# Performance work log

Measured on AMD Instinct MI355X. Metric: run time of the kernel, lower is better.

## Reference

```python
import jax, jax.numpy as jnp
import numpy as np

CHEB_K = 3

def setup_inputs() -> dict:
    key = jax.random.key(0)
    k1, k2, k3, k4 = jax.random.split(key, 4)
    B, N, C_IN, C_OUT, D = 64, 2048, 64, 64, 16
    return {
        "x": jax.random.normal(k1, (B, N, C_IN), dtype=jnp.float32),
        "node_embeddings": jax.random.normal(k2, (N, D), dtype=jnp.float32),
        "weights_pool": jax.random.normal(k3, (D, CHEB_K, C_IN, C_OUT), dtype=jnp.float32) * 0.1,
        "bias_pool": jax.random.normal(k4, (D, C_OUT), dtype=jnp.float32) * 0.1,
    }

def reference(x, node_embeddings, weights_pool, bias_pool):
    # x: [B, N, C_in]; node_embeddings: [N, D]
    N = node_embeddings.shape[0]
    # adaptive adjacency: row-softmax of relu(E E^T)
    supports = jax.nn.softmax(jax.nn.relu(node_embeddings @ node_embeddings.T), axis=1)
    # Chebyshev polynomial recursion: T0 = I, T1 = A, Tk = 2 A T_{k-1} - T_{k-2}
    support_set = [jnp.eye(N, dtype=x.dtype), supports]
    for _ in range(2, CHEB_K):
        support_set.append(2.0 * supports @ support_set[-1] - support_set[-2])
    supports_stack = jnp.stack(support_set, axis=0)  # [K, N, N]
    # per-node generated weights/bias from embedding pools
    weights = jnp.einsum('nd,dkio->nkio', node_embeddings, weights_pool)  # [N, K, C_in, C_out]
    bias = node_embeddings @ bias_pool  # [N, C_out]
    # graph convolution: aggregate then per-node GEMM
    x_g = jnp.einsum('knm,bmc->bknc', supports_stack, x)  # [B, K, N, C_in]
    out = jnp.einsum('bkni,nkio->bno', x_g, weights) + bias  # [B, N, C_out]
    return out
```

## Files before the change

kernel.cpp:

```cpp
#include <hip/hip_runtime.h>
#include <hip/hip_bf16.h>
#include <stdint.h>

using bf16   = __bf16;
using bf16x8 = __attribute__((ext_vector_type(8))) __bf16;
using f32x4  = __attribute__((ext_vector_type(4))) float;

#define NN  2048
#define DD  16
#define BB  64
#define CC  64
#define BCC 4096
#define GNODE 2

__device__ inline float4 f4max(float4 a, float4 b) {
  return make_float4(fmaxf(a.x,b.x), fmaxf(a.y,b.y), fmaxf(a.z,b.z), fmaxf(a.w,b.w));
}
__device__ inline float4 f4add(float4 a, float4 b) {
  return make_float4(a.x+b.x, a.y+b.y, a.z+b.z, a.w+b.w);
}

__global__ __launch_bounds__(256) void k_softmax(const float* __restrict__ E,
                                                 bf16* __restrict__ A) {
  const int n0 = blockIdx.x * 4;
  const int t = threadIdx.x;
  float en[4][DD];
#pragma unroll
  for (int g = 0; g < 4; ++g)
#pragma unroll
    for (int d = 0; d < DD; ++d) en[g][d] = E[(size_t)(n0 + g) * DD + d];

  float4 r[8];
  float4 mx = make_float4(0.f, 0.f, 0.f, 0.f);
#pragma unroll
  for (int j = 0; j < 8; ++j) {
    const int m = t + 256 * j;
    const float4* ep = (const float4*)(E + (size_t)m * DD);
    float4 p0 = ep[0], p1 = ep[1], p2 = ep[2], p3 = ep[3];
    float s[4];
#pragma unroll
    for (int g = 0; g < 4; ++g) {
      s[g] = p0.x*en[g][0] + p0.y*en[g][1] + p0.z*en[g][2] + p0.w*en[g][3]
           + p1.x*en[g][4] + p1.y*en[g][5] + p1.z*en[g][6] + p1.w*en[g][7]
           + p2.x*en[g][8] + p2.y*en[g][9] + p2.z*en[g][10] + p2.w*en[g][11]
           + p3.x*en[g][12]+ p3.y*en[g][13]+ p3.z*en[g][14]+ p3.w*en[g][15];
      s[g] = fmaxf(s[g], 0.0f);
    }
    r[j] = make_float4(s[0], s[1], s[2], s[3]);
    mx = f4max(mx, r[j]);
  }
  __shared__ float4 red[256];
  red[t] = mx;
  __syncthreads();
  for (int off = 128; off > 0; off >>= 1) {
    if (t < off) red[t] = f4max(red[t], red[t + off]);
    __syncthreads();
  }
  mx = red[0];
  __syncthreads();
  float4 ex[8];
  float4 sum = make_float4(0.f, 0.f, 0.f, 0.f);
#pragma unroll
  for (int j = 0; j < 8; ++j) {
    ex[j] = make_float4(__expf(r[j].x - mx.x), __expf(r[j].y - mx.y),
                        __expf(r[j].z - mx.z), __expf(r[j].w - mx.w));
    sum = f4add(sum, ex[j]);
  }
  red[t] = sum;
  __syncthreads();
  for (int off = 128; off > 0; off >>= 1) {
    if (t < off) red[t] = f4add(red[t], red[t + off]);
    __syncthreads();
  }
  const float4 tot = red[0];
  const float inv[4] = {1.f/tot.x, 1.f/tot.y, 1.f/tot.z, 1.f/tot.w};
#pragma unroll
  for (int j = 0; j < 8; ++j) {
    const int m = t + 256 * j;
    A[(size_t)(n0 + 0) * NN + m] = (bf16)(ex[j].x * inv[0]);
    A[(size_t)(n0 + 1) * NN + m] = (bf16)(ex[j].y * inv[1]);
    A[(size_t)(n0 + 2) * NN + m] = (bf16)(ex[j].z * inv[2]);
    A[(size_t)(n0 + 3) * NN + m] = (bf16)(ex[j].w * inv[3]);
  }
}

__global__ __launch_bounds__(256) void k_transpose(const bf16* __restrict__ in,
                                                   bf16* __restrict__ out,
                                                   int R, int C) {
  __shared__ bf16 tile[64 * 68];
  const int bx = blockIdx.x, by = blockIdx.y;
  const int t = threadIdx.x;
  const int r0 = by * 64, c0 = bx * 64;
#pragma unroll
  for (int j = 0; j < 16; ++j) {
    const int q = t + 256 * j;
    const int r = q >> 6, c = q & 63;
    tile[r * 68 + c] = in[(size_t)(r0 + r) * C + c0 + c];
  }
  __syncthreads();
#pragma unroll
  for (int j = 0; j < 16; ++j) {
    const int q = t + 256 * j;
    const int rr = q >> 6, cc = q & 63;
    out[(size_t)(c0 + rr) * R + r0 + cc] = tile[cc * 68 + rr];
  }
}

__global__ __launch_bounds__(256) void k_build_xrt(const float* __restrict__ x,
                                                   bf16* __restrict__ XrT) {
  __shared__ bf16 tile[64 * 68];
  const int b = blockIdx.x;
  const int m0 = blockIdx.y * 64;
  const int t = threadIdx.x;
#pragma unroll
  for (int j = 0; j < 16; ++j) {
    const int q = t + 256 * j;
    const int m = q >> 6, i = q & 63;
    tile[m * 68 + i] = (bf16)x[((size_t)b * NN + m0 + m) * CC + i];
  }
  __syncthreads();
#pragma unroll
  for (int j = 0; j < 16; ++j) {
    const int q = t + 256 * j;
    const int i = q >> 6, m = q & 63;
    XrT[((size_t)b * CC + i) * NN + m0 + m] = tile[m * 68 + i];
  }
}

__global__ __launch_bounds__(256) void k_prep_wpt(const float* __restrict__ Wp,
                                                  bf16* __restrict__ WpT) {
  const int e = blockIdx.x * 256 + threadIdx.x;
  const int r = e >> 6, o = e & 63;
  const size_t src = (size_t)(r >> 6) * 4096 + (size_t)(r & 63) * 64 + o;
#pragma unroll
  for (int d = 0; d < DD; ++d)
    WpT[(size_t)e * DD + d] = (bf16)Wp[(size_t)d * 12288 + src];
}

template <int EPI>
__global__ __launch_bounds__(256) void k_gemm_bt(const bf16* __restrict__ L,
                                                 const bf16* __restrict__ R,
                                                 bf16* __restrict__ C,
                                                 int M, int Nc, int K,
                                                 const float* __restrict__ Xext,
                                                 bf16* __restrict__ CT) {
  __shared__ uint4 lds[4096];
  const int t = threadIdx.x;
  const int lane = t & 63, w = t >> 6;
  const int wm = w & 1, wn = w >> 1;
  const int h = lane >> 4;

  const int nwg = gridDim.x * gridDim.y;
  const int bid = blockIdx.y * gridDim.x + blockIdx.x;
  const int cpx = nwg >> 3;
  const int swz = (bid & 7) * cpx + (bid >> 3);
  const int bx = swz % gridDim.x, by = swz / gridDim.x;

  const int m0 = by * 128, n0 = bx * 128;

  f32x4 acc[4][4];
  const f32x4 zz = {0.f, 0.f, 0.f, 0.f};
#pragma unroll
  for (int mt = 0; mt < 4; ++mt)
#pragma unroll
    for (int nt = 0; nt < 4; ++nt) acc[mt][nt] = zz;

  auto stage = [&](int buf, int kt) {
    uint4* base = lds + buf * 2048;
#pragma unroll
    for (int c = 0; c < 4; ++c) {
      const int q = t + 256 * c;
      const int row = q >> 3, col4 = q & 7;
      const int scol = col4 ^ (row & 7);
      const bf16* srcL = L + (size_t)(m0 + row) * K + kt + (scol << 3);
      const bf16* srcR = R + (size_t)(n0 + row) * K + kt + (scol << 3);
      __builtin_amdgcn_global_load_lds(srcL, &base[q & ~63], 16, 0, 0);
      __builtin_amdgcn_global_load_lds(srcR, &base[1024 + (q & ~63)], 16, 0, 0);
    }
  };

  auto compute = [&](int buf) {
    const bf16x8* Lsv = (const bf16x8*)(lds + buf * 2048);
    const bf16x8* Rsv = (const bf16x8*)(lds + buf * 2048 + 1024);
#pragma unroll
    for (int kk = 0; kk < 2; ++kk) {
      bf16x8 af[4], bfr[4];
#pragma unroll
      for (int mt = 0; mt < 4; ++mt) {
        const int row = wm * 64 + mt * 16 + (lane & 15);
        af[mt] = Lsv[(row << 3) | ((kk * 4 + h) ^ (row & 7))];
      }
#pragma unroll
      for (int nt = 0; nt < 4; ++nt) {
        const int row = wn * 64 + nt * 16 + (lane & 15);
        bfr[nt] = Rsv[(row << 3) | ((kk * 4 + h) ^ (row & 7))];
      }
#pragma unroll
      for (int mt = 0; mt < 4; ++mt)
#pragma unroll
        for (int nt = 0; nt < 4; ++nt)
          acc[mt][nt] = __builtin_amdgcn_mfma_f32_16x16x32_bf16(
              af[mt], bfr[nt], acc[mt][nt], 0, 0, 0);
    }
  };

  const int NT = K >> 6;
  stage(0, 0);
  int cur = 0;
  for (int ts = 0; ts < NT - 1; ++ts) {
    stage(cur ^ 1, (ts + 1) << 6);
    asm volatile("s_waitcnt vmcnt(8)" ::: "memory");
    __builtin_amdgcn_s_barrier();
    __builtin_amdgcn_sched_barrier(0);
    compute(cur);
    __builtin_amdgcn_s_barrier();
    __builtin_amdgcn_sched_barrier(0);
    cur ^= 1;
  }
  asm volatile("s_waitcnt vmcnt(0)" ::: "memory");
  __builtin_amdgcn_s_barrier();
  __builtin_amdgcn_sched_barrier(0);
  compute(cur);

#pragma unroll
  for (int mt = 0; mt < 4; ++mt)
#pragma unroll
    for (int nt = 0; nt < 4; ++nt)
#pragma unroll
      for (int r = 0; r < 4; ++r) {
        const int rg = m0 + wm * 64 + mt * 16 + 4 * h + r;
        const int cg = n0 + wn * 64 + nt * 16 + (lane & 15);
        float v = acc[mt][nt][r];
        if (EPI == 2) {
          const int b = cg >> 6, i = cg & 63;
          v = 2.0f * v - Xext[(((size_t)b * NN + rg) * CC) + i];
        }
        C[(size_t)rg * Nc + cg] = (bf16)v;
      }

  if (EPI == 1) {
    __syncthreads();
    bf16* T = (bf16*)lds;
#pragma unroll
    for (int mt = 0; mt < 4; ++mt)
#pragma unroll
      for (int nt = 0; nt < 4; ++nt)
#pragma unroll
        for (int r = 0; r < 4; ++r) {
          const int rloc = wm * 64 + mt * 16 + 4 * h + r;
          const int cloc = wn * 64 + nt * 16 + (lane & 15);
          T[cloc * 136 + rloc] = (bf16)acc[mt][nt][r];
        }
    __syncthreads();
    const int cloc = t >> 1, half = t & 1;
#pragma unroll
    for (int jj = 0; jj < 8; ++jj) {
      const bf16x8 v = *(const bf16x8*)(T + cloc * 136 + half * 64 + jj * 8);
      *(bf16x8*)(CT + (size_t)(n0 + cloc) * M + m0 + half * 64 + jj * 8) = v;
    }
  }
}

__global__ __launch_bounds__(256) void k_node(const float* __restrict__ x,
                                              const float* __restrict__ E,
                                              const bf16* __restrict__ WpT,
                                              const float* __restrict__ bp,
                                              const bf16* __restrict__ xg1,
                                              const bf16* __restrict__ xg2,
                                              float* __restrict__ out) {
  __shared__ alignas(16) bf16 sW[GNODE * 1536 * 8];
  const int t = threadIdx.x;
  const int lane = t & 63, w = t >> 6;
  const int h = lane >> 4, l16 = lane & 15;
  const int n0 = blockIdx.x * GNODE;
  const int b = w * 16 + l16;

  float4  xa[GNODE][4];
  bf16x8  xgr[GNODE][4];
#pragma unroll
  for (int g = 0; g < GNODE; ++g) {
    const int n = n0 + g;
    const float* xb = x + ((size_t)b * NN + n) * CC;
    xa[g][0] = *(const float4*)(xb + h * 8);
    xa[g][1] = *(const float4*)(xb + h * 8 + 4);
    xa[g][2] = *(const float4*)(xb + 32 + h * 8);
    xa[g][3] = *(const float4*)(xb + 32 + h * 8 + 4);
    const bf16* x1 = xg1 + (size_t)n * BCC + b * CC;
    const bf16* x2 = xg2 + (size_t)n * BCC + b * CC;
    xgr[g][0] = *(const bf16x8*)(x1 + h * 8);
    xgr[g][1] = *(const bf16x8*)(x1 + 32 + h * 8);
    xgr[g][2] = *(const bf16x8*)(x2 + h * 8);
    xgr[g][3] = *(const bf16x8*)(x2 + 32 + h * 8);
  }

  float en[GNODE][DD];
#pragma unroll
  for (int g = 0; g < GNODE; ++g)
#pragma unroll
    for (int d = 0; d < DD; ++d) en[g][d] = E[(size_t)(n0 + g) * DD + d];

  float bias_v[GNODE][4];
#pragma unroll
  for (int g = 0; g < GNODE; ++g)
#pragma unroll
    for (int nt = 0; nt < 4; ++nt) {
      const int o = nt * 16 + l16;
      float a = 0.0f;
#pragma unroll
      for (int d = 0; d < DD; ++d) a += en[g][d] * bp[d * CC + o];
      bias_v[g][nt] = a;
    }

#pragma unroll
  for (int c = 0; c < 6; ++c) {
    const int idx = t + 256 * c;
    const int o = idx & 63;
    const int u = idx >> 6;
    const bf16* src = WpT + ((size_t)(u * 8) * 64 + o) * DD;
    bf16x8 wv[GNODE];
#pragma unroll
    for (int j = 0; j < 8; ++j) {
      const bf16x8* wr = (const bf16x8*)(src + (size_t)j * 64 * DD);
      bf16x8 w0 = wr[0], w1 = wr[1];
      float wf[DD];
#pragma unroll
      for (int d = 0; d < 8; ++d) { wf[d] = (float)w0[d]; wf[8 + d] = (float)w1[d]; }
#pragma unroll
      for (int g = 0; g < GNODE; ++g) {
        float a = 0.0f;
#pragma unroll
        for (int d = 0; d < DD; ++d) a += en[g][d] * wf[d];
        wv[g][j] = (bf16)a;
      }
    }
    const int swz = o * 24 + (u & ~7) + ((u & 7) ^ (o & 7));
#pragma unroll
    for (int g = 0; g < GNODE; ++g)
      *(bf16x8*)(sW + (size_t)(g * 1536 + swz) * 8) = wv[g];
  }
  __syncthreads();

#pragma unroll
  for (int g = 0; g < GNODE; ++g) {
    f32x4 acc[4];
    const f32x4 zz = {0.f, 0.f, 0.f, 0.f};
#pragma unroll
    for (int nt = 0; nt < 4; ++nt) acc[nt] = zz;
#pragma unroll
    for (int s = 0; s < 6; ++s) {
      bf16x8 af;
      if (s < 2) {
        const float4 u4 = xa[g][s * 2], v4 = xa[g][s * 2 + 1];
        af[0] = (bf16)u4.x; af[1] = (bf16)u4.y; af[2] = (bf16)u4.z; af[3] = (bf16)u4.w;
        af[4] = (bf16)v4.x; af[5] = (bf16)v4.y; af[6] = (bf16)v4.z; af[7] = (bf16)v4.w;
      } else {
        af = xgr[g][s - 2];
      }
      const int u = s * 4 + h;
#pragma unroll
      for (int nt = 0; nt < 4; ++nt) {
        const int o = nt * 16 + l16;
        const bf16x8 bfr = *(const bf16x8*)(
            sW + (size_t)(g * 1536 + o * 24 + (u & ~7) + ((u & 7) ^ (o & 7))) * 8);
        acc[nt] = __builtin_amdgcn_mfma_f32_16x16x32_bf16(af, bfr, acc[nt], 0, 0, 0);
      }
    }
#pragma unroll
    for (int nt = 0; nt < 4; ++nt) {
      const int o = nt * 16 + l16;
#pragma unroll
      for (int r = 0; r < 4; ++r) {
        const int br = w * 16 + 4 * h + r;
        out[((size_t)br * NN + (n0 + g)) * CC + o] = acc[nt][r] + bias_v[g][nt];
      }
    }
  }
}

extern "C" void kernel_launch(void* const* d_in, const int* in_sizes, int n_in,
                              void* d_out, int out_size, void* d_ws, size_t ws_size,
                              hipStream_t stream) {
  const float* x  = (const float*)d_in[0];
  const float* E  = (const float*)d_in[1];
  const float* Wp = (const float*)d_in[2];
  const float* bp = (const float*)d_in[3];
  float* out = (float*)d_out;

  char* ws = (char*)d_ws;
  const size_t MB = (size_t)1 << 20;
  bf16* A    = (bf16*)(ws);
  bf16* XrT  = (bf16*)(ws + 8 * MB);
  bf16* xg1  = (bf16*)(ws + 24 * MB);
  bf16* xg2  = (bf16*)(ws + 40 * MB);
  bf16* WpT  = (bf16*)(ws + 56 * MB);

  k_softmax<<<NN / 4, 256, 0, stream>>>(E, A);
  k_build_xrt<<<dim3(64, 32), 256, 0, stream>>>(x, XrT);
  k_prep_wpt<<<48, 256, 0, stream>>>(Wp, WpT);

  if (ws_size >= 80 * MB) {
    bf16* Xg1T = (bf16*)(ws + 60 * MB);
    k_gemm_bt<1><<<dim3(32, 16), 256, 0, stream>>>(A, XrT, xg1, NN, BCC, NN,
                                                   nullptr, Xg1T);
    k_gemm_bt<2><<<dim3(32, 16), 256, 0, stream>>>(A, Xg1T, xg2, NN, BCC, NN,
                                                   x, nullptr);
  } else {
    bf16* Xg1T = XrT;
    k_gemm_bt<0><<<dim3(32, 16), 256, 0, stream>>>(A, XrT, xg1, NN, BCC, NN,
                                                   nullptr, nullptr);
    k_transpose<<<dim3(64, 32), 256, 0, stream>>>(xg1, Xg1T, NN, BCC);
    k_gemm_bt<2><<<dim3(32, 16), 256, 0, stream>>>(A, Xg1T, xg2, NN, BCC, NN,
                                                   x, nullptr);
  }
  k_node<<<NN / GNODE, 256, 0, stream>>>(x, E, WpT, bp, xg1, xg2, out);
}
```

Baseline: 149.0 us.

## Remap GEMM tiles per XCD into 8x8 blocks and split node kernel across 512 threads

The GEMM block-index swizzle now gives each XCD a contiguous 8x8 tile region for the 32x16 grid, so tiles sharing the same L operand rows and R columns land on the same L2. The node kernel goes from 256 to 512 threads: each group of 4 waves handles one of the two nodes instead of one wave looping over both. This halves per-thread weight generation and register pressure and exposes more parallelism. The cost is larger blocks, which may limit occupancy.

New measurement: 149.7 us. No clear change (+0.4%).

```diff
diff --git a/kernel.cpp b/kernel.cpp
--- a/kernel.cpp
+++ b/kernel.cpp
@@ -152,9 +152,17 @@
 
   const int nwg = gridDim.x * gridDim.y;
   const int bid = blockIdx.y * gridDim.x + blockIdx.x;
-  const int cpx = nwg >> 3;
-  const int swz = (bid & 7) * cpx + (bid >> 3);
-  const int bx = swz % gridDim.x, by = swz / gridDim.x;
+  int bx, by;
+  if (gridDim.x == 32 && gridDim.y == 16) {
+    const int xcd = bid & 7, j = bid >> 3;
+    bx = (xcd & 3) * 8 + (j & 7);
+    by = (xcd >> 2) * 8 + (j >> 3);
+  } else {
+    const int cpx = nwg >> 3;
+    const int swz = (bid & 7) * cpx + (bid >> 3);
+    bx = swz % gridDim.x;
+    by = swz / gridDim.x;
+  }
 
   const int m0 = by * 128, n0 = bx * 128;
 
@@ -261,7 +269,7 @@
   }
 }
 
-__global__ __launch_bounds__(256) void k_node(const float* __restrict__ x,
+__global__ __launch_bounds__(512) void k_node(const float* __restrict__ x,
                                               const float* __restrict__ E,
                                               const bf16* __restrict__ WpT,
                                               const float* __restrict__ bp,
@@ -272,48 +280,46 @@
   const int t = threadIdx.x;
   const int lane = t & 63, w = t >> 6;
   const int h = lane >> 4, l16 = lane & 15;
+  const int wl = w & 3, g = w >> 2;
   const int n0 = blockIdx.x * GNODE;
-  const int b = w * 16 + l16;
-
-  float4  xa[GNODE][4];
-  bf16x8  xgr[GNODE][4];
-#pragma unroll
-  for (int g = 0; g < GNODE; ++g) {
-    const int n = n0 + g;
+  const int n = n0 + g;
+  const int b = wl * 16 + l16;
+
+  float4 xa[4];
+  bf16x8 xgr[4];
+  {
     const float* xb = x + ((size_t)b * NN + n) * CC;
-    xa[g][0] = *(const float4*)(xb + h * 8);
-    xa[g][1] = *(const float4*)(xb + h * 8 + 4);
-    xa[g][2] = *(const float4*)(xb + 32 + h * 8);
-    xa[g][3] = *(const float4*)(xb + 32 + h * 8 + 4);
+    xa[0] = *(const float4*)(xb + h * 8);
+    xa[1] = *(const float4*)(xb + h * 8 + 4);
+    xa[2] = *(const float4*)(xb + 32 + h * 8);
+    xa[3] = *(const float4*)(xb + 32 + h * 8 + 4);
     const bf16* x1 = xg1 + (size_t)n * BCC + b * CC;
     const bf16* x2 = xg2 + (size_t)n * BCC + b * CC;
-    xgr[g][0] = *(const bf16x8*)(x1 + h * 8);
-    xgr[g][1] = *(const bf16x8*)(x1 + 32 + h * 8);
-    xgr[g][2] = *(const bf16x8*)(x2 + h * 8);
-    xgr[g][3] = *(const bf16x8*)(x2 + 32 + h * 8);
+    xgr[0] = *(const bf16x8*)(x1 + h * 8);
+    xgr[1] = *(const bf16x8*)(x1 + 32 + h * 8);
+    xgr[2] = *(const bf16x8*)(x2 + h * 8);
+    xgr[3] = *(const bf16x8*)(x2 + 32 + h * 8);
   }
 
   float en[GNODE][DD];
 #pragma unroll
-  for (int g = 0; g < GNODE; ++g)
-#pragma unroll
-    for (int d = 0; d < DD; ++d) en[g][d] = E[(size_t)(n0 + g) * DD + d];
-
-  float bias_v[GNODE][4];
-#pragma unroll
-  for (int g = 0; g < GNODE; ++g)
-#pragma unroll
-    for (int nt = 0; nt < 4; ++nt) {
-      const int o = nt * 16 + l16;
-      float a = 0.0f;
-#pragma unroll
-      for (int d = 0; d < DD; ++d) a += en[g][d] * bp[d * CC + o];
-      bias_v[g][nt] = a;
-    }
-
-#pragma unroll
-  for (int c = 0; c < 6; ++c) {
-    const int idx = t + 256 * c;
+  for (int gg = 0; gg < GNODE; ++gg)
+#pragma unroll
+    for (int d = 0; d < DD; ++d) en[gg][d] = E[(size_t)(n0 + gg) * DD + d];
+
+  float bias_v[4];
+#pragma unroll
+  for (int nt = 0; nt < 4; ++nt) {
+    const int o = nt * 16 + l16;
+    float a = 0.0f;
+#pragma unroll
+    for (int d = 0; d < DD; ++d) a += en[g][d] * bp[d * CC + o];
+    bias_v[nt] = a;
+  }
+
+#pragma unroll
+  for (int c = 0; c < 3; ++c) {
+    const int idx = t + 512 * c;
     const int o = idx & 63;
     const int u = idx >> 6;
     const bf16* src = WpT + ((size_t)(u * 8) * 64 + o) * DD;
@@ -326,53 +332,51 @@
 #pragma unroll
       for (int d = 0; d < 8; ++d) { wf[d] = (float)w0[d]; wf[8 + d] = (float)w1[d]; }
 #pragma unroll
-      for (int g = 0; g < GNODE; ++g) {
+      for (int gg = 0; gg < GNODE; ++gg) {
         float a = 0.0f;
 #pragma unroll
-        for (int d = 0; d < DD; ++d) a += en[g][d] * wf[d];
-        wv[g][j] = (bf16)a;
+        for (int d = 0; d < DD; ++d) a += en[gg][d] * wf[d];
+        wv[gg][j] = (bf16)a;
       }
     }
     const int swz = o * 24 + (u & ~7) + ((u & 7) ^ (o & 7));
 #pragma unroll
-    for (int g = 0; g < GNODE; ++g)
-      *(bf16x8*)(sW + (size_t)(g * 1536 + swz) * 8) = wv[g];
-  }
-  __syncthreads();
-
-#pragma unroll
-  for (int g = 0; g < GNODE; ++g) {
-    f32x4 acc[4];
-    const f32x4 zz = {0.f, 0.f, 0.f, 0.f};
-#pragma unroll
-    for (int nt = 0; nt < 4; ++nt) acc[nt] = zz;
-#pragma unroll
-    for (int s = 0; s < 6; ++s) {
-      bf16x8 af;
-      if (s < 2) {
-        const float4 u4 = xa[g][s * 2], v4 = xa[g][s * 2 + 1];
-        af[0] = (bf16)u4.x; af[1] = (bf16)u4.y; af[2] = (bf16)u4.z; af[3] = (bf16)u4.w;
-        af[4] = (bf16)v4.x; af[5] = (bf16)v4.y; af[6] = (bf16)v4.z; af[7] = (bf16)v4.w;
-      } else {
-        af = xgr[g][s - 2];
-      }
-      const int u = s * 4 + h;
-#pragma unroll
-      for (int nt = 0; nt < 4; ++nt) {
-        const int o = nt * 16 + l16;
-        const bf16x8 bfr = *(const bf16x8*)(
-            sW + (size_t)(g * 1536 + o * 24 + (u & ~7) + ((u & 7) ^ (o & 7))) * 8);
-        acc[nt] = __builtin_amdgcn_mfma_f32_16x16x32_bf16(af, bfr, acc[nt], 0, 0, 0);
-      }
-    }
+    for (int gg = 0; gg < GNODE; ++gg)
+      *(bf16x8*)(sW + (size_t)(gg * 1536 + swz) * 8) = wv[gg];
+  }
+  __syncthreads();
+
+  f32x4 acc[4];
+  const f32x4 zz = {0.f, 0.f, 0.f, 0.f};
+#pragma unroll
+  for (int nt = 0; nt < 4; ++nt) acc[nt] = zz;
+
+#pragma unroll
+  for (int s = 0; s < 6; ++s) {
+    bf16x8 af;
+    if (s < 2) {
+      const float4 u4 = xa[s * 2], v4 = xa[s * 2 + 1];
+      af[0] = (bf16)u4.x; af[1] = (bf16)u4.y; af[2] = (bf16)u4.z; af[3] = (bf16)u4.w;
+      af[4] = (bf16)v4.x; af[5] = (bf16)v4.y; af[6] = (bf16)v4.z; af[7] = (bf16)v4.w;
+    } else {
+      af = xgr[s - 2];
+    }
+    const int u = s * 4 + h;
 #pragma unroll
     for (int nt = 0; nt < 4; ++nt) {
       const int o = nt * 16 + l16;
-#pragma unroll
-      for (int r = 0; r < 4; ++r) {
-        const int br = w * 16 + 4 * h + r;
-        out[((size_t)br * NN + (n0 + g)) * CC + o] = acc[nt][r] + bias_v[g][nt];
-      }
+      const bf16x8 bfr = *(const bf16x8*)(
+          sW + (size_t)(g * 1536 + o * 24 + (u & ~7) + ((u & 7) ^ (o & 7))) * 8);
+      acc[nt] = __builtin_amdgcn_mfma_f32_16x16x32_bf16(af, bfr, acc[nt], 0, 0, 0);
+    }
+  }
+#pragma unroll
+  for (int nt = 0; nt < 4; ++nt) {
+    const int o = nt * 16 + l16;
+#pragma unroll
+    for (int r = 0; r < 4; ++r) {
+      const int br = wl * 16 + 4 * h + r;
+      out[((size_t)br * NN + n) * CC + o] = acc[nt][r] + bias_v[nt];
     }
   }
 }
@@ -412,5 +416,5 @@
     k_gemm_bt<2><<<dim3(32, 16), 256, 0, stream>>>(A, Xg1T, xg2, NN, BCC, NN,
                                                    x, nullptr);
   }
-  k_node<<<NN / GNODE, 256, 0, stream>>>(x, E, WpT, bp, xg1, xg2, out);
-}
+  k_node<<<NN / GNODE, 512, 0, stream>>>(x, E, WpT, bp, xg1, xg2, out);
+}
```
